# Kernel optimization log

Measured on AMD Instinct MI355X. Metric: run time of the kernel, lower is better.

## Reference

```python
import jax, jax.numpy as jnp
import numpy as np

N_SRC, N_DST, E = 100000, 10000, 320000
F_IN, HID, NCLS = 128, 256, 3
NEG_SLOPE = 0.2


def setup_inputs() -> dict:
    key = jax.random.key(0)
    ks = jax.random.split(key, 10)
    return {
        "x_src": jax.random.normal(ks[0], (N_SRC, F_IN), jnp.float32),
        "x_dst": jax.random.normal(ks[1], (N_DST, F_IN), jnp.float32),
        "edge_src": jax.random.randint(ks[2], (E,), 0, N_SRC),
        "edge_dst": jax.random.randint(ks[3], (E,), 0, N_DST),
        "W": jax.random.normal(ks[4], (F_IN, HID), jnp.float32) * (1.0 / np.sqrt(F_IN)),
        "att_src": jax.random.normal(ks[5], (HID,), jnp.float32) * 0.1,
        "att_dst": jax.random.normal(ks[6], (HID,), jnp.float32) * 0.1,
        "bias": jnp.zeros((HID,), jnp.float32),
        "Wc": jax.random.normal(ks[7], (HID, NCLS), jnp.float32) * (1.0 / np.sqrt(HID)),
        "bc": jnp.zeros((NCLS,), jnp.float32),
    }


def reference(x_src, x_dst, edge_src, edge_dst, W, att_src, att_dst, bias, Wc, bc):
    # Linear transform (heads=1, out=256)
    h_src = x_src @ W                      # [N_src, H]
    h_dst = x_dst @ W                      # [N_dst, H]
    # Per-node attention contributions, then gather per edge
    a_src = h_src @ att_src                # [N_src]
    a_dst = h_dst @ att_dst                # [N_dst]
    logits = jax.nn.leaky_relu(a_dst[edge_dst] + a_src[edge_src], NEG_SLOPE)  # [E]
    # Segment softmax over incoming edges of each destination node
    m = jax.ops.segment_max(logits, edge_dst, num_segments=N_DST)
    e = jnp.exp(logits - m[edge_dst])
    denom = jax.ops.segment_sum(e, edge_dst, num_segments=N_DST) + 1e-16
    alpha = e / denom[edge_dst]            # [E]
    # Weighted scatter-sum of source messages
    out = jax.ops.segment_sum(alpha[:, None] * h_src[edge_src], edge_dst, num_segments=N_DST)
    out = out + bias                       # [N_dst, H]
    scores = out @ Wc + bc                 # [N_dst, 3]
    return jax.nn.log_softmax(scores, axis=1)
```

## Files before the change

kernel.cpp:

```cpp
#include <hip/hip_runtime.h>
#include <float.h>

#define NSRC 100000
#define NDST 10000
#define NEDGE 320000
#define FIN 128
#define HID 256
#define NCLS 3
#define NEG_SLOPE 0.2f

#define RANGES 4
#define REPL 64
#define DPB (NDST / RANGES)
#define EPB (NEDGE / REPL)
#define TPB 512

__global__ void prep_kernel(const float* __restrict__ W, const float* __restrict__ att_src,
                            const float* __restrict__ att_dst, const float* __restrict__ bias,
                            const float* __restrict__ Wc, const float* __restrict__ bc,
                            float* __restrict__ wa_src, float* __restrict__ wa_dst,
                            float* __restrict__ wfc, float* __restrict__ bf) {
  int l = threadIdx.x;
  if (blockIdx.x < FIN) {
    int k = blockIdx.x;
    float4 w = ((const float4*)(W + (size_t)k * HID))[l];
    int h0 = 4 * l;
    float s1 = w.x * att_src[h0] + w.y * att_src[h0 + 1] + w.z * att_src[h0 + 2] + w.w * att_src[h0 + 3];
    float s2 = w.x * att_dst[h0] + w.y * att_dst[h0 + 1] + w.z * att_dst[h0 + 2] + w.w * att_dst[h0 + 3];
    float f0 = w.x * Wc[h0 * NCLS] + w.y * Wc[(h0 + 1) * NCLS] + w.z * Wc[(h0 + 2) * NCLS] + w.w * Wc[(h0 + 3) * NCLS];
    float f1 = w.x * Wc[h0 * NCLS + 1] + w.y * Wc[(h0 + 1) * NCLS + 1] + w.z * Wc[(h0 + 2) * NCLS + 1] + w.w * Wc[(h0 + 3) * NCLS + 1];
    float f2 = w.x * Wc[h0 * NCLS + 2] + w.y * Wc[(h0 + 1) * NCLS + 2] + w.z * Wc[(h0 + 2) * NCLS + 2] + w.w * Wc[(h0 + 3) * NCLS + 2];
#pragma unroll
    for (int off = 32; off; off >>= 1) {
      s1 += __shfl_down(s1, off);
      s2 += __shfl_down(s2, off);
      f0 += __shfl_down(f0, off);
      f1 += __shfl_down(f1, off);
      f2 += __shfl_down(f2, off);
    }
    if (l == 0) {
      wa_src[k] = s1;
      wa_dst[k] = s2;
      wfc[0 * FIN + k] = f0;
      wfc[1 * FIN + k] = f1;
      wfc[2 * FIN + k] = f2;
    }
  } else {
    float b0 = 0.f, b1 = 0.f, b2 = 0.f;
#pragma unroll
    for (int j = 0; j < 4; ++j) {
      int h = l + 64 * j;
      float bi = bias[h];
      b0 += bi * Wc[h * NCLS + 0];
      b1 += bi * Wc[h * NCLS + 1];
      b2 += bi * Wc[h * NCLS + 2];
    }
#pragma unroll
    for (int off = 32; off; off >>= 1) {
      b0 += __shfl_down(b0, off);
      b1 += __shfl_down(b1, off);
      b2 += __shfl_down(b2, off);
    }
    if (l == 0) {
      bf[0] = b0 + bc[0];
      bf[1] = b1 + bc[1];
      bf[2] = b2 + bc[2];
    }
  }
}

__global__ void matvec_fused_kernel(const float* __restrict__ x_src, const float* __restrict__ x_dst,
                                    const float* __restrict__ wa_src, const float* __restrict__ wa_dst,
                                    const float* __restrict__ wfc, float* __restrict__ a_src,
                                    float* __restrict__ a_dst, float4* __restrict__ q4) {
  int gid = blockIdx.x * blockDim.x + threadIdx.x;
  int row = gid >> 5;
  int l = threadIdx.x & 31;
  if (row < NSRC) {
    float4 v = ((const float4*)(x_src + (size_t)row * FIN))[l];
    float4 w = ((const float4*)wa_src)[l];
    float4 c0 = ((const float4*)(wfc + 0 * FIN))[l];
    float4 c1 = ((const float4*)(wfc + 1 * FIN))[l];
    float4 c2 = ((const float4*)(wfc + 2 * FIN))[l];
    float p0 = v.x * w.x + v.y * w.y + v.z * w.z + v.w * w.w;
    float p1 = v.x * c0.x + v.y * c0.y + v.z * c0.z + v.w * c0.w;
    float p2 = v.x * c1.x + v.y * c1.y + v.z * c1.z + v.w * c1.w;
    float p3 = v.x * c2.x + v.y * c2.y + v.z * c2.z + v.w * c2.w;
#pragma unroll
    for (int off = 16; off; off >>= 1) {
      p0 += __shfl_down(p0, off);
      p1 += __shfl_down(p1, off);
      p2 += __shfl_down(p2, off);
      p3 += __shfl_down(p3, off);
    }
    if (l == 0) {
      a_src[row] = p0;
      q4[row] = make_float4(p1, p2, p3, 1.0f);
    }
  } else {
    int rd = row - NSRC;
    if (rd >= NDST) return;
    float4 v = ((const float4*)(x_dst + (size_t)rd * FIN))[l];
    float4 w = ((const float4*)wa_dst)[l];
    float p = v.x * w.x + v.y * w.y + v.z * w.z + v.w * w.w;
#pragma unroll
    for (int off = 16; off; off >>= 1) p += __shfl_down(p, off);
    if (l == 0) a_dst[rd] = p;
  }
}

__global__ __launch_bounds__(TPB) void edge_lds_kernel(
    const int* __restrict__ edge_src, const int* __restrict__ edge_dst,
    const float* __restrict__ a_src, const float* __restrict__ a_dst,
    const float4* __restrict__ q4, float* __restrict__ partial) {
  __shared__ float lacc[DPB * 4];
  int c = blockIdx.x;
  int r = blockIdx.y;
  int tid = threadIdx.x;
  for (int i = tid; i < DPB * 4; i += TPB) lacc[i] = 0.f;
  __syncthreads();

  int d0 = r * DPB;
  int ebase = c * EPB;
  for (int i = tid; i < EPB; i += TPB) {
    int e = ebase + i;
    int d = edge_dst[e];
    unsigned dr = (unsigned)(d - d0);
    if (dr < (unsigned)DPB) {
      int s = edge_src[e];
      float z = a_dst[d] + a_src[s];
      float logit = (z >= 0.f) ? z : NEG_SLOPE * z;
      float w = __expf(logit);
      float4 qv = q4[s];
      float* b = lacc + dr * 4;
      atomicAdd(b + 0, w * qv.x);
      atomicAdd(b + 1, w * qv.y);
      atomicAdd(b + 2, w * qv.z);
      atomicAdd(b + 3, w);
    }
  }
  __syncthreads();

  float* dst = partial + ((size_t)r * REPL + c) * (DPB * 4);
  for (int i = tid; i < DPB * 4; i += TPB) dst[i] = lacc[i];
}

__global__ void merge_finalize_kernel(const float4* __restrict__ partial,
                                      const float* __restrict__ bf, float* __restrict__ out) {
  int d = blockIdx.x * blockDim.x + threadIdx.x;
  if (d >= NDST) return;
  int r = d / DPB;
  int dr = d - r * DPB;
  const float4* base = partial + (size_t)r * REPL * DPB + dr;
  float a0 = 0.f, a1 = 0.f, a2 = 0.f, aw = 0.f;
#pragma unroll 4
  for (int c = 0; c < REPL; ++c) {
    float4 v = base[(size_t)c * DPB];
    a0 += v.x;
    a1 += v.y;
    a2 += v.z;
    aw += v.w;
  }
  float inv = 1.f / (aw + 1e-16f);
  float s0 = a0 * inv + bf[0];
  float s1 = a1 * inv + bf[1];
  float s2 = a2 * inv + bf[2];
  float mx = fmaxf(s0, fmaxf(s1, s2));
  float l = logf(__expf(s0 - mx) + __expf(s1 - mx) + __expf(s2 - mx));
  out[d * NCLS + 0] = s0 - mx - l;
  out[d * NCLS + 1] = s1 - mx - l;
  out[d * NCLS + 2] = s2 - mx - l;
}

extern "C" void kernel_launch(void* const* d_in, const int* in_sizes, int n_in,
                              void* d_out, int out_size, void* d_ws, size_t ws_size,
                              hipStream_t stream) {
  const float* x_src    = (const float*)d_in[0];
  const float* x_dst    = (const float*)d_in[1];
  const int*   edge_src = (const int*)d_in[2];
  const int*   edge_dst = (const int*)d_in[3];
  const float* W        = (const float*)d_in[4];
  const float* att_src  = (const float*)d_in[5];
  const float* att_dst  = (const float*)d_in[6];
  const float* bias     = (const float*)d_in[7];
  const float* Wc       = (const float*)d_in[8];
  const float* bc       = (const float*)d_in[9];
  float* out = (float*)d_out;

  char* p = (char*)d_ws;
  auto carve = [&](size_t bytes) {
    void* r = (void*)p;
    p += (bytes + 255) & ~(size_t)255;
    return r;
  };
  float*  wa_src  = (float*)carve(FIN * 4);
  float*  wa_dst  = (float*)carve(FIN * 4);
  float*  wfc     = (float*)carve(NCLS * FIN * 4);
  float*  bf      = (float*)carve(NCLS * 4);
  float*  a_src   = (float*)carve((size_t)NSRC * 4);
  float*  a_dst   = (float*)carve((size_t)NDST * 4);
  float4* q4      = (float4*)carve((size_t)NSRC * 16);
  float*  partial = (float*)carve((size_t)RANGES * REPL * DPB * 4 * 4);

  prep_kernel<<<FIN + 1, 64, 0, stream>>>(W, att_src, att_dst, bias, Wc, bc,
                                          wa_src, wa_dst, wfc, bf);
  {
    int rows = NSRC + NDST;
    int blocks = (rows * 32 + 255) / 256;
    matvec_fused_kernel<<<blocks, 256, 0, stream>>>(x_src, x_dst, wa_src, wa_dst, wfc,
                                                    a_src, a_dst, q4);
  }
  edge_lds_kernel<<<dim3(REPL, RANGES), TPB, 0, stream>>>(edge_src, edge_dst, a_src, a_dst,
                                                          q4, partial);
  merge_finalize_kernel<<<(NDST + 255) / 256, 256, 0, stream>>>((const float4*)partial, bf, out);
}
```

Measured before the change: 129.6 us.

## Fuse edge scatter and merge-finalize into one kernel with atomic completion counter

Merges the edge accumulation kernel and the merge/finalize kernel into a single launch. Extra blocks spin on a global done counter until all edge blocks have published their partials, then reduce with four threads per destination and an LDS combine. It also packs a_src into the w lane of q4, which saves one gather per edge, stages a_dst in LDS, and raises block size to 1024. The spin-wait relies on the edge blocks being scheduled before the merge blocks, which risks deadlock or idle CUs while the merge blocks wait.

Result: slower. 229.7 us (+77.3%).

```diff
diff --git a/kernel.cpp b/kernel.cpp
--- a/kernel.cpp
+++ b/kernel.cpp
@@ -13,7 +13,9 @@
 #define REPL 64
 #define DPB (NDST / RANGES)
 #define EPB (NEDGE / REPL)
-#define TPB 512
+#define TPB 1024
+#define NEBLK (RANGES * REPL)
+#define NMBLK 40
 
 __global__ void prep_kernel(const float* __restrict__ W, const float* __restrict__ att_src,
                             const float* __restrict__ att_dst, const float* __restrict__ bias,
@@ -71,8 +73,9 @@
 
 __global__ void matvec_fused_kernel(const float* __restrict__ x_src, const float* __restrict__ x_dst,
                                     const float* __restrict__ wa_src, const float* __restrict__ wa_dst,
-                                    const float* __restrict__ wfc, float* __restrict__ a_src,
-                                    float* __restrict__ a_dst, float4* __restrict__ q4) {
+                                    const float* __restrict__ wfc, float* __restrict__ a_dst,
+                                    float4* __restrict__ q4, int* __restrict__ done) {
+  if (blockIdx.x == 0 && threadIdx.x == 0) *done = 0;
   int gid = blockIdx.x * blockDim.x + threadIdx.x;
   int row = gid >> 5;
   int l = threadIdx.x & 31;
@@ -93,10 +96,7 @@
       p2 += __shfl_down(p2, off);
       p3 += __shfl_down(p3, off);
     }
-    if (l == 0) {
-      a_src[row] = p0;
-      q4[row] = make_float4(p1, p2, p3, 1.0f);
-    }
+    if (l == 0) q4[row] = make_float4(p1, p2, p3, p0);
   } else {
     int rd = row - NSRC;
     if (rd >= NDST) return;
@@ -109,67 +109,95 @@
   }
 }
 
-__global__ __launch_bounds__(TPB) void edge_lds_kernel(
+__global__ __launch_bounds__(TPB) void edge_merge_kernel(
     const int* __restrict__ edge_src, const int* __restrict__ edge_dst,
-    const float* __restrict__ a_src, const float* __restrict__ a_dst,
-    const float4* __restrict__ q4, float* __restrict__ partial) {
-  __shared__ float lacc[DPB * 4];
-  int c = blockIdx.x;
-  int r = blockIdx.y;
+    const float* __restrict__ a_dst, const float4* __restrict__ q4,
+    float4* __restrict__ partial, int* __restrict__ done,
+    const float* __restrict__ bf, float* __restrict__ out) {
+  __shared__ float smem[DPB * 4 + DPB];
+  int b = blockIdx.x;
   int tid = threadIdx.x;
-  for (int i = tid; i < DPB * 4; i += TPB) lacc[i] = 0.f;
-  __syncthreads();
-
-  int d0 = r * DPB;
-  int ebase = c * EPB;
-  for (int i = tid; i < EPB; i += TPB) {
-    int e = ebase + i;
-    int d = edge_dst[e];
-    unsigned dr = (unsigned)(d - d0);
-    if (dr < (unsigned)DPB) {
-      int s = edge_src[e];
-      float z = a_dst[d] + a_src[s];
-      float logit = (z >= 0.f) ? z : NEG_SLOPE * z;
-      float w = __expf(logit);
-      float4 qv = q4[s];
-      float* b = lacc + dr * 4;
-      atomicAdd(b + 0, w * qv.x);
-      atomicAdd(b + 1, w * qv.y);
-      atomicAdd(b + 2, w * qv.z);
-      atomicAdd(b + 3, w);
-    }
-  }
-  __syncthreads();
-
-  float* dst = partial + ((size_t)r * REPL + c) * (DPB * 4);
-  for (int i = tid; i < DPB * 4; i += TPB) dst[i] = lacc[i];
-}
-
-__global__ void merge_finalize_kernel(const float4* __restrict__ partial,
-                                      const float* __restrict__ bf, float* __restrict__ out) {
-  int d = blockIdx.x * blockDim.x + threadIdx.x;
-  if (d >= NDST) return;
-  int r = d / DPB;
-  int dr = d - r * DPB;
-  const float4* base = partial + (size_t)r * REPL * DPB + dr;
-  float a0 = 0.f, a1 = 0.f, a2 = 0.f, aw = 0.f;
+
+  if (b < NEBLK) {
+    float* lacc = smem;
+    float* ladst = smem + DPB * 4;
+    int c = b & (REPL - 1);
+    int r = b >> 6;
+    int d0 = r * DPB;
+    for (int i = tid; i < DPB * 4; i += TPB) lacc[i] = 0.f;
+    for (int i = tid; i < DPB; i += TPB) ladst[i] = a_dst[d0 + i];
+    __syncthreads();
+
+    int ebase = c * EPB;
+    for (int i = tid; i < EPB; i += TPB) {
+      int e = ebase + i;
+      int d = edge_dst[e];
+      unsigned dr = (unsigned)(d - d0);
+      if (dr < (unsigned)DPB) {
+        int s = edge_src[e];
+        float4 qv = q4[s];
+        float z = ladst[dr] + qv.w;
+        float logit = (z >= 0.f) ? z : NEG_SLOPE * z;
+        float w = __expf(logit);
+        float* bp = lacc + dr * 4;
+        atomicAdd(bp + 0, w * qv.x);
+        atomicAdd(bp + 1, w * qv.y);
+        atomicAdd(bp + 2, w * qv.z);
+        atomicAdd(bp + 3, w);
+      }
+    }
+    __syncthreads();
+
+    float4* dst = partial + (size_t)b * DPB;
+    float4* lv = (float4*)lacc;
+    for (int i = tid; i < DPB; i += TPB) dst[i] = lv[i];
+    __threadfence();
+    __syncthreads();
+    if (tid == 0) atomicAdd(done, 1);
+  } else {
+    if (tid == 0) {
+      while (__hip_atomic_load(done, __ATOMIC_ACQUIRE, __HIP_MEMORY_SCOPE_AGENT) < NEBLK) {}
+    }
+    __syncthreads();
+    __threadfence();
+
+    int mt = (b - NEBLK) * TPB + tid;
+    int d = mt >> 2;
+    int slot = mt & 3;
+    float4* red = (float4*)smem;
+    float4 acc = make_float4(0.f, 0.f, 0.f, 0.f);
+    if (d < NDST) {
+      int r = d / DPB;
+      int dr = d - r * DPB;
+      const float4* base = partial + (size_t)(r * REPL) * DPB + dr;
 #pragma unroll 4
-  for (int c = 0; c < REPL; ++c) {
-    float4 v = base[(size_t)c * DPB];
-    a0 += v.x;
-    a1 += v.y;
-    a2 += v.z;
-    aw += v.w;
-  }
-  float inv = 1.f / (aw + 1e-16f);
-  float s0 = a0 * inv + bf[0];
-  float s1 = a1 * inv + bf[1];
-  float s2 = a2 * inv + bf[2];
-  float mx = fmaxf(s0, fmaxf(s1, s2));
-  float l = logf(__expf(s0 - mx) + __expf(s1 - mx) + __expf(s2 - mx));
-  out[d * NCLS + 0] = s0 - mx - l;
-  out[d * NCLS + 1] = s1 - mx - l;
-  out[d * NCLS + 2] = s2 - mx - l;
+      for (int c = slot * (REPL / 4); c < (slot + 1) * (REPL / 4); ++c) {
+        float4 v = base[(size_t)c * DPB];
+        acc.x += v.x;
+        acc.y += v.y;
+        acc.z += v.z;
+        acc.w += v.w;
+      }
+    }
+    red[tid] = acc;
+    __syncthreads();
+    if (slot == 0 && d < NDST) {
+      float4 v0 = red[tid], v1 = red[tid + 1], v2 = red[tid + 2], v3 = red[tid + 3];
+      float a0 = v0.x + v1.x + v2.x + v3.x;
+      float a1 = v0.y + v1.y + v2.y + v3.y;
+      float a2 = v0.z + v1.z + v2.z + v3.z;
+      float aw = v0.w + v1.w + v2.w + v3.w;
+      float inv = 1.f / (aw + 1e-16f);
+      float s0 = a0 * inv + bf[0];
+      float s1 = a1 * inv + bf[1];
+      float s2 = a2 * inv + bf[2];
+      float mx = fmaxf(s0, fmaxf(s1, s2));
+      float l = logf(__expf(s0 - mx) + __expf(s1 - mx) + __expf(s2 - mx));
+      out[d * NCLS + 0] = s0 - mx - l;
+      out[d * NCLS + 1] = s1 - mx - l;
+      out[d * NCLS + 2] = s2 - mx - l;
+    }
+  }
 }
 
 extern "C" void kernel_launch(void* const* d_in, const int* in_sizes, int n_in,
@@ -197,10 +225,10 @@
   float*  wa_dst  = (float*)carve(FIN * 4);
   float*  wfc     = (float*)carve(NCLS * FIN * 4);
   float*  bf      = (float*)carve(NCLS * 4);
-  float*  a_src   = (float*)carve((size_t)NSRC * 4);
   float*  a_dst   = (float*)carve((size_t)NDST * 4);
   float4* q4      = (float4*)carve((size_t)NSRC * 16);
-  float*  partial = (float*)carve((size_t)RANGES * REPL * DPB * 4 * 4);
+  int*    done    = (int*)carve(256);
+  float4* partial = (float4*)carve((size_t)NEBLK * DPB * 16);
 
   prep_kernel<<<FIN + 1, 64, 0, stream>>>(W, att_src, att_dst, bias, Wc, bc,
                                           wa_src, wa_dst, wfc, bf);
@@ -208,9 +236,8 @@
     int rows = NSRC + NDST;
     int blocks = (rows * 32 + 255) / 256;
     matvec_fused_kernel<<<blocks, 256, 0, stream>>>(x_src, x_dst, wa_src, wa_dst, wfc,
-                                                    a_src, a_dst, q4);
-  }
-  edge_lds_kernel<<<dim3(REPL, RANGES), TPB, 0, stream>>>(edge_src, edge_dst, a_src, a_dst,
-                                                          q4, partial);
-  merge_finalize_kernel<<<(NDST + 255) / 256, 256, 0, stream>>>((const float4*)partial, bf, out);
-}
+                                                    a_dst, q4, done);
+  }
+  edge_merge_kernel<<<NEBLK + NMBLK, TPB, 0, stream>>>(edge_src, edge_dst, a_dst, q4,
+                                                       partial, done, bf, out);
+}
```
